# Kernel optimization log

Measured on AMD Instinct MI355X. Metric: run time of the kernel, lower is better.

The kernel has to match this reference:

```python
import jax, jax.numpy as jnp
import numpy as np

N_NODES = 100000


def gcn_conv(x, edge_index, W, b):
    """PyG GCNConv: h = x W^T; add self-loops; symmetric deg^-1/2 norm; scatter-add; + bias."""
    n = x.shape[0]
    src = jnp.concatenate([edge_index[0], jnp.arange(n)])  # self-loops appended
    dst = jnp.concatenate([edge_index[1], jnp.arange(n)])
    deg = jax.ops.segment_sum(jnp.ones_like(dst, dtype=x.dtype), dst, num_segments=n)
    dinv = jnp.where(deg > 0, jax.lax.rsqrt(deg), 0.0)
    norm = dinv[src] * dinv[dst]                             # [E+n]
    h = x @ W.T                                              # [n, out]
    msg = norm[:, None] * h[src]                             # [E+n, out] gather
    out = jax.ops.segment_sum(msg, dst, num_segments=n)      # scatter-add
    return out + b


def setup_inputs() -> dict:
    key = jax.random.key(0)
    ks = jax.random.split(key, 10)
    input_dim, gnn_hidden, tree_hidden, num_classes = 128, 64, 32, 8
    n_edges = 3200000
    x = jax.random.normal(ks[0], (N_NODES, input_dim), dtype=jnp.float32)
    edge_index = jax.random.randint(ks[1], (2, n_edges), 0, N_NODES, dtype=jnp.int64)
    # GCNConv params (PyG Linear weight is [out, in], glorot-ish scale)
    W1 = jax.random.normal(ks[2], (gnn_hidden, input_dim), dtype=jnp.float32) / np.sqrt(input_dim)
    b1 = jnp.zeros((gnn_hidden,), dtype=jnp.float32)
    W2 = jax.random.normal(ks[3], (tree_hidden, gnn_hidden), dtype=jnp.float32) / np.sqrt(gnn_hidden)
    b2 = jnp.zeros((tree_hidden,), dtype=jnp.float32)
    # SoftDecisionTree params (torch.randn init in source)
    gate_w = jax.random.normal(ks[4], (tree_hidden, tree_hidden), dtype=jnp.float32)
    gate_b = jnp.zeros((tree_hidden,), dtype=jnp.float32)
    leaf_w = jax.random.normal(ks[5], (tree_hidden, num_classes), dtype=jnp.float32)
    return {"x": x, "edge_index": edge_index, "W1": W1, "b1": b1, "W2": W2,
            "b2": b2, "gate_w": gate_w, "gate_b": gate_b, "leaf_w": leaf_w}


def reference(x, edge_index, W1, b1, W2, b2, gate_w, gate_b, leaf_w):
    h = jax.nn.relu(gcn_conv(x, edge_index, W1, b1))
    h = gcn_conv(h, edge_index, W2, b2)
    gates = jax.nn.sigmoid(h @ gate_w.T + gate_b)
    return gates @ leaf_w
```

## Files before the change

### kernel.cpp

```cpp
#include <hip/hip_runtime.h>
#include <math.h>

#define IN_DIM 128
#define H1 64
#define H2 32
#define NC 8
#define SCAN_CH 1024
#define NB_MAX 512
#define BLK 512
#define CAP 12288

typedef unsigned int u32;

__device__ __forceinline__ float bf_lo(u32 u) { return __uint_as_float(u << 16); }
__device__ __forceinline__ float bf_hi(u32 u) { return __uint_as_float(u & 0xffff0000u); }
__device__ __forceinline__ unsigned short f2b(float f) {
  u32 u = __float_as_uint(f);
  u += 0x7fffu + ((u >> 16) & 1u);
  return (unsigned short)(u >> 16);
}


__global__ __launch_bounds__(256) void k_hist(const int* __restrict__ dst,
                                              int* __restrict__ bh,
                                              int E, int EPB, int NBk) {
  __shared__ int h[NB_MAX];
  int k = blockIdx.x, tid = threadIdx.x;
  for (int i = tid; i < NBk; i += 256) h[i] = 0;
  __syncthreads();
  int st = k * EPB, en = min(E, st + EPB);
  for (int i = st + tid; i < en; i += 256)
    atomicAdd(&h[((u32)dst[i]) >> 8], 1);
  __syncthreads();
  for (int b = tid; b < NBk; b += 256) bh[b * BLK + k] = h[b];
}


__global__ __launch_bounds__(256) void k_gsc1(const int* __restrict__ A,
                                              int* __restrict__ bsum, int L) {
  int b = blockIdx.x, tid = threadIdx.x;
  int i0 = b * SCAN_CH + tid * 4;
  int s = 0;
  if (i0 + 3 < L) {
    int4 v = *(const int4*)(A + i0);
    s = v.x + v.y + v.z + v.w;
  } else {
    for (int i = i0; i < L; ++i) s += A[i];
  }
  __shared__ int red[256];
  red[tid] = s;
  __syncthreads();
  for (int d = 128; d > 0; d >>= 1) {
    if (tid < d) red[tid] += red[tid + d];
    __syncthreads();
  }
  if (tid == 0) bsum[b] = red[0];
}

__global__ __launch_bounds__(256) void k_gsc2(const int* __restrict__ bsum,
                                              int* __restrict__ bbase,
                                              int* __restrict__ S, int nbk, int L) {
  __shared__ int part[256];
  int tid = threadIdx.x;
  int chunk = (nbk + 255) / 256;
  int st = tid * chunk, en = min(st + chunk, nbk);
  int s = 0;
  for (int i = st; i < en; ++i) s += bsum[i];
  part[tid] = s;
  __syncthreads();
  for (int d = 1; d < 256; d <<= 1) {
    int t = (tid >= d) ? part[tid - d] : 0;
    __syncthreads();
    part[tid] += t;
    __syncthreads();
  }
  int base = (tid == 0) ? 0 : part[tid - 1];
  for (int i = st; i < en; ++i) { bbase[i] = base; base += bsum[i]; }
  if (tid == 255) S[L] = part[255];
}

__global__ __launch_bounds__(256) void k_gsc3(const int* __restrict__ A,
                                              const int* __restrict__ bbase,
                                              int* __restrict__ S, int L) {
  int b = blockIdx.x, tid = threadIdx.x;
  int i0 = b * SCAN_CH + tid * 4;
  int e0 = 0, e1 = 0, e2 = 0, e3 = 0;
  if (i0 + 3 < L) {
    int4 v = *(const int4*)(A + i0);
    e0 = v.x; e1 = v.y; e2 = v.z; e3 = v.w;
  } else {
    if (i0 + 0 < L) e0 = A[i0 + 0];
    if (i0 + 1 < L) e1 = A[i0 + 1];
    if (i0 + 2 < L) e2 = A[i0 + 2];
    if (i0 + 3 < L) e3 = A[i0 + 3];
  }
  __shared__ int part[256];
  part[tid] = e0 + e1 + e2 + e3;
  __syncthreads();
  for (int d = 1; d < 256; d <<= 1) {
    int t = (tid >= d) ? part[tid - d] : 0;
    __syncthreads();
    part[tid] += t;
    __syncthreads();
  }
  int base = bbase[b] + ((tid == 0) ? 0 : part[tid - 1]);
  int o0 = base, o1 = o0 + e0, o2 = o1 + e1, o3 = o2 + e2;
  if (i0 + 3 < L) {
    int4 o; o.x = o0; o.y = o1; o.z = o2; o.w = o3;
    *(int4*)(S + i0) = o;
  } else {
    if (i0 + 0 < L) S[i0 + 0] = o0;
    if (i0 + 1 < L) S[i0 + 1] = o1;
    if (i0 + 2 < L) S[i0 + 2] = o2;
    if (i0 + 3 < L) S[i0 + 3] = o3;
  }
}


__global__ __launch_bounds__(256) void k_scatter(const int* __restrict__ src,
                                                 const int* __restrict__ dst,
                                                 const int* __restrict__ S,
                                                 u32* __restrict__ packed,
                                                 int E, int EPB, int NBk) {
  __shared__ int cur[NB_MAX];
  int k = blockIdx.x, tid = threadIdx.x;
  for (int b = tid; b < NBk; b += 256) cur[b] = S[b * BLK + k];
  __syncthreads();
  int st = k * EPB, en = min(E, st + EPB);
  for (int i = st + tid; i < en; i += 256) {
    int d = dst[i];
    int b = ((u32)d) >> 8;
    int pos = atomicAdd(&cur[b], 1);
    packed[pos] = (((u32)d & 255u) << 17) | (u32)src[i];
  }
}


__global__ __launch_bounds__(256) void k_build(const u32* __restrict__ packed,
                                               const int* __restrict__ S,
                                               int* __restrict__ csr,
                                               int* __restrict__ off,
                                               float* __restrict__ dinv,
                                               int n, int NBk) {
  __shared__ int cnt[256];
  __shared__ int tmp[256];
  __shared__ int cur[256];
  __shared__ int sbuf[CAP];
  int b = blockIdx.x, tid = threadIdx.x;
  int r0 = S[b * BLK];
  int r1 = S[(b + 1) * BLK];
  int m = r1 - r0;
  cnt[tid] = 0;
  __syncthreads();
  for (int i = r0 + tid; i < r1; i += 256)
    atomicAdd(&cnt[packed[i] >> 17], 1);
  __syncthreads();
  int v = cnt[tid];
  tmp[tid] = v;
  __syncthreads();
  for (int d = 1; d < 256; d <<= 1) {
    int t = (tid >= d) ? tmp[tid - d] : 0;
    __syncthreads();
    tmp[tid] += t;
    __syncthreads();
  }
  int rel = tmp[tid] - v;
  int node = b * 256 + tid;
  if (node < n) {
    off[node] = r0 + rel;
    dinv[node] = rsqrtf((float)(v + 1));
  }
  if (b == NBk - 1 && tid == 0) off[n] = r1;
  cur[tid] = rel;
  __syncthreads();
  if (m <= CAP) {
    for (int i = r0 + tid; i < r1; i += 256) {
      u32 u = packed[i];
      int pos = atomicAdd(&cur[u >> 17], 1);
      sbuf[pos] = (int)(u & 0x1FFFFu);
    }
    __syncthreads();
    for (int j = tid; j < m; j += 256)
      csr[r0 + j] = sbuf[j];
  } else {
    for (int i = r0 + tid; i < r1; i += 256) {
      u32 u = packed[i];
      int pos = atomicAdd(&cur[u >> 17], 1);
      csr[r0 + pos] = (int)(u & 0x1FFFFu);
    }
  }
}


__global__ void k_proj1(const float4* __restrict__ x4, const float* __restrict__ W1,
                        const float* __restrict__ dinv,
                        unsigned short* __restrict__ h1p, int n) {
  __shared__ float xs[16][IN_DIM];
  __shared__ float wt[IN_DIM][H1 + 1];
  int tid = threadIdx.x;
  int row0 = blockIdx.x * 16;

  for (int i = tid; i < (H1 * IN_DIM / 4); i += 256) {
    float4 w = ((const float4*)W1)[i];
    int o = (i * 4) / IN_DIM;
    int k = (i * 4) % IN_DIM;
    wt[k + 0][o] = w.x; wt[k + 1][o] = w.y; wt[k + 2][o] = w.z; wt[k + 3][o] = w.w;
  }
  for (int i = tid; i < 16 * IN_DIM / 4; i += 256) {
    int r = (i * 4) / IN_DIM, k = (i * 4) % IN_DIM;
    int row = row0 + r;
    if (row < n)
      *((float4*)&xs[r][k]) = x4[(size_t)row * (IN_DIM / 4) + k / 4];
  }
  __syncthreads();

  int o = tid & 63, rq = tid >> 6;
  float a0 = 0.f, a1 = 0.f, a2 = 0.f, a3 = 0.f;
  for (int k = 0; k < IN_DIM; ++k) {
    float w = wt[k][o];
    a0 += xs[rq * 4 + 0][k] * w;
    a1 += xs[rq * 4 + 1][k] * w;
    a2 += xs[rq * 4 + 2][k] * w;
    a3 += xs[rq * 4 + 3][k] * w;
  }
  int r = row0 + rq * 4;
  if (r + 0 < n) h1p[(size_t)(r + 0) * H1 + o] = f2b(a0 * dinv[r + 0]);
  if (r + 1 < n) h1p[(size_t)(r + 1) * H1 + o] = f2b(a1 * dinv[r + 1]);
  if (r + 2 < n) h1p[(size_t)(r + 2) * H1 + o] = f2b(a2 * dinv[r + 2]);
  if (r + 3 < n) h1p[(size_t)(r + 3) * H1 + o] = f2b(a3 * dinv[r + 3]);
}


__global__ __launch_bounds__(256) void k_agg64_proj2(
    const u32* __restrict__ hp,
    const float* __restrict__ dinv,
    const int* __restrict__ off, const int* __restrict__ csr,
    const float* __restrict__ b1, const float* __restrict__ W2,
    unsigned short* __restrict__ h2p, int n) {
  __shared__ float wt[H1][H2 + 1];
  __shared__ float rows[4][H1];
  int tid = threadIdx.x;

  for (int i = tid; i < H2 * H1 / 4; i += 256) {
    float4 w = ((const float4*)W2)[i];
    int o = (i * 4) / H1, k = (i * 4) % H1;
    wt[k + 0][o] = w.x; wt[k + 1][o] = w.y; wt[k + 2][o] = w.z; wt[k + 3][o] = w.w;
  }

  int lane = tid & 63;
  int wv = __builtin_amdgcn_readfirstlane(tid >> 6);
  int wid0 = blockIdx.x * 4 + wv;
  int wid = wid0 < n ? wid0 : n - 1;
  int half = lane >> 5, f2 = lane & 31;

  float ax = 0.f, ay = 0.f;
  if (half == 0) {
    u32 u = hp[(size_t)wid * (H1 / 2) + f2];
    ax = bf_lo(u); ay = bf_hi(u);
  }
  int r0 = off[wid], r1 = off[wid + 1];
  int i = r0 + half;
  for (; i + 6 < r1; i += 8) {
    int s0 = csr[i + 0], s1 = csr[i + 2], s2 = csr[i + 4], s3 = csr[i + 6];
    u32 u0 = hp[(size_t)s0 * (H1 / 2) + f2];
    u32 u1 = hp[(size_t)s1 * (H1 / 2) + f2];
    u32 u2 = hp[(size_t)s2 * (H1 / 2) + f2];
    u32 u3 = hp[(size_t)s3 * (H1 / 2) + f2];
    ax += bf_lo(u0); ay += bf_hi(u0);
    ax += bf_lo(u1); ay += bf_hi(u1);
    ax += bf_lo(u2); ay += bf_hi(u2);
    ax += bf_lo(u3); ay += bf_hi(u3);
  }
  for (; i < r1; i += 2) {
    u32 u = hp[(size_t)csr[i] * (H1 / 2) + f2];
    ax += bf_lo(u);
    ay += bf_hi(u);
  }
  ax += __shfl_down(ax, 32, 64);
  ay += __shfl_down(ay, 32, 64);
  float d = dinv[wid];
  if (half == 0) {
    float2 rv;
    rv.x = fmaxf(ax * d + b1[2 * f2 + 0], 0.f);
    rv.y = fmaxf(ay * d + b1[2 * f2 + 1], 0.f);
    *(float2*)&rows[wv][2 * f2] = rv;
  }
  __syncthreads();

  int o = lane & 31;
  float a = 0.f;
#pragma unroll
  for (int k = 0; k < 32; ++k) {
    int kk = half * 32 + k;
    a += rows[wv][kk] * wt[kk][o];
  }
  a += __shfl_down(a, 32, 64);
  if (half == 0 && wid0 < n) h2p[(size_t)wid0 * H2 + o] = f2b(a * d);
}


__global__ __launch_bounds__(256) void k_agg32_tree(
    const u32* __restrict__ hp,
    const float* __restrict__ dinv,
    const int* __restrict__ off, const int* __restrict__ csr,
    const float* __restrict__ b2, const float* __restrict__ gate_w,
    const float* __restrict__ gate_b, const float* __restrict__ leaf_w,
    float* __restrict__ out, int n) {
  __shared__ float gwt[H2][H2 + 1];
  __shared__ float lws[H2][NC + 1];
  __shared__ float rowh[4][H2];
  __shared__ float rowg[4][H2];
  int tid = threadIdx.x;

  {
    float4 w = ((const float4*)gate_w)[tid];
    int j = (tid * 4) / H2, k = (tid * 4) % H2;
    gwt[k + 0][j] = w.x; gwt[k + 1][j] = w.y; gwt[k + 2][j] = w.z; gwt[k + 3][j] = w.w;
  }
  lws[tid >> 3][tid & 7] = leaf_w[tid];

  int lane = tid & 63;
  int wv = __builtin_amdgcn_readfirstlane(tid >> 6);
  int wid0 = blockIdx.x * 4 + wv;
  int wid = wid0 < n ? wid0 : n - 1;
  int q = lane >> 4, f2 = lane & 15;

  float ax = 0.f, ay = 0.f;
  if (q == 0) {
    u32 u = hp[(size_t)wid * (H2 / 2) + f2];
    ax = bf_lo(u); ay = bf_hi(u);
  }
  int r0 = off[wid], r1 = off[wid + 1];
  int i = r0 + q;
  for (; i + 12 < r1; i += 16) {
    int s0 = csr[i + 0], s1 = csr[i + 4], s2 = csr[i + 8], s3 = csr[i + 12];
    u32 u0 = hp[(size_t)s0 * (H2 / 2) + f2];
    u32 u1 = hp[(size_t)s1 * (H2 / 2) + f2];
    u32 u2 = hp[(size_t)s2 * (H2 / 2) + f2];
    u32 u3 = hp[(size_t)s3 * (H2 / 2) + f2];
    ax += bf_lo(u0); ay += bf_hi(u0);
    ax += bf_lo(u1); ay += bf_hi(u1);
    ax += bf_lo(u2); ay += bf_hi(u2);
    ax += bf_lo(u3); ay += bf_hi(u3);
  }
  for (; i < r1; i += 4) {
    u32 u = hp[(size_t)csr[i] * (H2 / 2) + f2];
    ax += bf_lo(u);
    ay += bf_hi(u);
  }
  ax += __shfl_down(ax, 32, 64); ay += __shfl_down(ay, 32, 64);
  ax += __shfl_down(ax, 16, 64); ay += __shfl_down(ay, 16, 64);
  float d = dinv[wid];
  if (lane < 16) {
    float2 rv;
    rv.x = ax * d + b2[2 * f2 + 0];
    rv.y = ay * d + b2[2 * f2 + 1];
    *(float2*)&rowh[wv][2 * f2] = rv;
  }
  __syncthreads();

  int half = lane >> 5, f = lane & 31;
  float g = 0.f;
#pragma unroll
  for (int k = 0; k < 16; ++k) {
    int kk = half * 16 + k;
    g += rowh[wv][kk] * gwt[kk][f];
  }
  g += __shfl_down(g, 32, 64);
  if (half == 0) rowg[wv][f] = 1.0f / (1.0f + __expf(-(g + gate_b[f])));
  __syncthreads();

  int c = lane & 7, gi = lane >> 3;
  float a = 0.f;
#pragma unroll
  for (int j4 = 0; j4 < 4; ++j4) {
    int jj = gi * 4 + j4;
    a += rowg[wv][jj] * lws[jj][c];
  }
  a += __shfl_down(a, 32, 64);
  a += __shfl_down(a, 16, 64);
  a += __shfl_down(a, 8, 64);
  if (lane < 8 && wid0 < n) out[(size_t)wid0 * NC + lane] = a;
}


extern "C" void kernel_launch(void* const* d_in, const int* in_sizes, int n_in,
                              void* d_out, int out_size, void* d_ws, size_t ws_size,
                              hipStream_t stream) {
  const float* x  = (const float*)d_in[0];
  const int*   ei = (const int*)d_in[1];
  const float* W1 = (const float*)d_in[2];
  const float* b1 = (const float*)d_in[3];
  const float* W2 = (const float*)d_in[4];
  const float* b2 = (const float*)d_in[5];
  const float* gw = (const float*)d_in[6];
  const float* gb = (const float*)d_in[7];
  const float* lw = (const float*)d_in[8];
  float* out = (float*)d_out;

  int n = in_sizes[0] / IN_DIM;
  int E = in_sizes[1] / 2;
  const int* src  = ei;
  const int* dstp = ei + E;

  int NBk = (n + 255) >> 8;
  int EPB = (E + BLK - 1) / BLK;
  int L   = NBk * BLK;
  int nbs = (L + SCAN_CH - 1) / SCAN_CH;

  size_t n4  = ((size_t)n + 3) & ~(size_t)3;
  size_t np4 = ((size_t)n + 1 + 3) & ~(size_t)3;
  size_t E4  = ((size_t)E + 3) & ~(size_t)3;
  size_t L4  = ((size_t)L + 1 + 3) & ~(size_t)3;
  size_t nbs4 = ((size_t)nbs + 3) & ~(size_t)3;
  char* w = (char*)d_ws;
  int* csr    = (int*)w;   w += E4 * 4;
  u32* packed = (u32*)w;   w += E4 * 4;
  int* bh     = (int*)w;   w += L4 * 4;
  int* S      = (int*)w;   w += L4 * 4;
  int* bsum   = (int*)w;   w += nbs4 * 4;
  int* bbase  = (int*)w;   w += nbs4 * 4;
  float* dinv = (float*)w; w += n4 * 4;
  int* off    = (int*)w;   w += np4 * 4;
  unsigned short* h1p = (unsigned short*)w;  w += n4 * (size_t)H1 * 2;
  unsigned short* h2p = (unsigned short*)w;

  int gw4 = (n + 3) / 4;

  k_hist<<<BLK, 256, 0, stream>>>(dstp, bh, E, EPB, NBk);
  k_gsc1<<<nbs, 256, 0, stream>>>(bh, bsum, L);
  k_gsc2<<<1, 256, 0, stream>>>(bsum, bbase, S, nbs, L);
  k_gsc3<<<nbs, 256, 0, stream>>>(bh, bbase, S, L);
  k_scatter<<<BLK, 256, 0, stream>>>(src, dstp, S, packed, E, EPB, NBk);
  k_build<<<NBk, 256, 0, stream>>>(packed, S, csr, off, dinv, n, NBk);

  k_proj1<<<(n + 15) / 16, 256, 0, stream>>>((const float4*)x, W1, dinv, h1p, n);
  k_agg64_proj2<<<gw4, 256, 0, stream>>>((const u32*)h1p, dinv, off, csr, b1, W2, h2p, n);
  k_agg32_tree<<<gw4, 256, 0, stream>>>((const u32*)h2p, dinv, off, csr, b2, gw, gb, lw, out, n);
}
```

Before: 415.7 us.

## Use 16-byte gathers and wave-cooperative CSR index loads in aggregation kernels

```diff
diff --git a/kernel.cpp b/kernel.cpp
--- a/kernel.cpp
+++ b/kernel.cpp
@@ -231,6 +231,18 @@
 }
 
 
+#define ACC8(v) do { \
+    a0 += bf_lo((v).x); a1 += bf_hi((v).x); \
+    a2 += bf_lo((v).y); a3 += bf_hi((v).y); \
+    a4 += bf_lo((v).z); a5 += bf_hi((v).z); \
+    a6 += bf_lo((v).w); a7 += bf_hi((v).w); } while (0)
+
+#define RED8(m) do { \
+    a0 += __shfl_xor(a0, m, 64); a1 += __shfl_xor(a1, m, 64); \
+    a2 += __shfl_xor(a2, m, 64); a3 += __shfl_xor(a3, m, 64); \
+    a4 += __shfl_xor(a4, m, 64); a5 += __shfl_xor(a5, m, 64); \
+    a6 += __shfl_xor(a6, m, 64); a7 += __shfl_xor(a7, m, 64); } while (0)
+
 __global__ __launch_bounds__(256) void k_agg64_proj2(
     const u32* __restrict__ hp,
     const float* __restrict__ dinv,
@@ -239,6 +251,7 @@
     unsigned short* __restrict__ h2p, int n) {
   __shared__ float wt[H1][H2 + 1];
   __shared__ float rows[4][H1];
+  __shared__ float b1s[H1];
   int tid = threadIdx.x;
 
   for (int i = tid; i < H2 * H1 / 4; i += 256) {
@@ -246,48 +259,55 @@
     int o = (i * 4) / H1, k = (i * 4) % H1;
     wt[k + 0][o] = w.x; wt[k + 1][o] = w.y; wt[k + 2][o] = w.z; wt[k + 3][o] = w.w;
   }
+  if (tid < 16) ((float4*)b1s)[tid] = ((const float4*)b1)[tid];
+  __syncthreads();
 
   int lane = tid & 63;
   int wv = __builtin_amdgcn_readfirstlane(tid >> 6);
   int wid0 = blockIdx.x * 4 + wv;
   int wid = wid0 < n ? wid0 : n - 1;
-  int half = lane >> 5, f2 = lane & 31;
-
-  float ax = 0.f, ay = 0.f;
-  if (half == 0) {
-    u32 u = hp[(size_t)wid * (H1 / 2) + f2];
-    ax = bf_lo(u); ay = bf_hi(u);
+  int g = lane >> 3, j = lane & 7;
+
+  const uint4* __restrict__ hp4 = (const uint4*)hp;
+  float a0 = 0.f, a1 = 0.f, a2 = 0.f, a3 = 0.f,
+        a4 = 0.f, a5 = 0.f, a6 = 0.f, a7 = 0.f;
+
+  if (g == 0) {
+    uint4 v = hp4[(size_t)wid * (H1 / 8) + j];
+    ACC8(v);
   }
   int r0 = off[wid], r1 = off[wid + 1];
-  int i = r0 + half;
-  for (; i + 6 < r1; i += 8) {
-    int s0 = csr[i + 0], s1 = csr[i + 2], s2 = csr[i + 4], s3 = csr[i + 6];
-    u32 u0 = hp[(size_t)s0 * (H1 / 2) + f2];
-    u32 u1 = hp[(size_t)s1 * (H1 / 2) + f2];
-    u32 u2 = hp[(size_t)s2 * (H1 / 2) + f2];
-    u32 u3 = hp[(size_t)s3 * (H1 / 2) + f2];
-    ax += bf_lo(u0); ay += bf_hi(u0);
-    ax += bf_lo(u1); ay += bf_hi(u1);
-    ax += bf_lo(u2); ay += bf_hi(u2);
-    ax += bf_lo(u3); ay += bf_hi(u3);
-  }
-  for (; i < r1; i += 2) {
-    u32 u = hp[(size_t)csr[i] * (H1 / 2) + f2];
-    ax += bf_lo(u);
-    ay += bf_hi(u);
-  }
-  ax += __shfl_down(ax, 32, 64);
-  ay += __shfl_down(ay, 32, 64);
+  for (int base = r0; base < r1; base += 32) {
+    int ci = base + (lane & 31);
+    int s = csr[min(ci, r1 - 1)];
+#pragma unroll
+    for (int it = 0; it < 4; ++it) {
+      int sv = __shfl(s, it * 8 + g, 64);
+      if (base + it * 8 + g < r1) {
+        uint4 v = hp4[(size_t)sv * (H1 / 8) + j];
+        ACC8(v);
+      }
+    }
+  }
+  RED8(8); RED8(16); RED8(32);
+
   float d = dinv[wid];
-  if (half == 0) {
-    float2 rv;
-    rv.x = fmaxf(ax * d + b1[2 * f2 + 0], 0.f);
-    rv.y = fmaxf(ay * d + b1[2 * f2 + 1], 0.f);
-    *(float2*)&rows[wv][2 * f2] = rv;
-  }
-  __syncthreads();
-
-  int o = lane & 31;
+  if (lane < 8) {
+    float4 v0, v1;
+    v0.x = fmaxf(a0 * d + b1s[8 * lane + 0], 0.f);
+    v0.y = fmaxf(a1 * d + b1s[8 * lane + 1], 0.f);
+    v0.z = fmaxf(a2 * d + b1s[8 * lane + 2], 0.f);
+    v0.w = fmaxf(a3 * d + b1s[8 * lane + 3], 0.f);
+    v1.x = fmaxf(a4 * d + b1s[8 * lane + 4], 0.f);
+    v1.y = fmaxf(a5 * d + b1s[8 * lane + 5], 0.f);
+    v1.z = fmaxf(a6 * d + b1s[8 * lane + 6], 0.f);
+    v1.w = fmaxf(a7 * d + b1s[8 * lane + 7], 0.f);
+    *(float4*)&rows[wv][8 * lane + 0] = v0;
+    *(float4*)&rows[wv][8 * lane + 4] = v1;
+  }
+  __syncthreads();
+
+  int half = lane >> 5, o = lane & 31;
   float a = 0.f;
 #pragma unroll
   for (int k = 0; k < 32; ++k) {
@@ -310,64 +330,72 @@
   __shared__ float lws[H2][NC + 1];
   __shared__ float rowh[4][H2];
   __shared__ float rowg[4][H2];
+  __shared__ float b2s[H2];
   int tid = threadIdx.x;
 
   {
     float4 w = ((const float4*)gate_w)[tid];
-    int j = (tid * 4) / H2, k = (tid * 4) % H2;
-    gwt[k + 0][j] = w.x; gwt[k + 1][j] = w.y; gwt[k + 2][j] = w.z; gwt[k + 3][j] = w.w;
+    int jj = (tid * 4) / H2, k = (tid * 4) % H2;
+    gwt[k + 0][jj] = w.x; gwt[k + 1][jj] = w.y; gwt[k + 2][jj] = w.z; gwt[k + 3][jj] = w.w;
   }
   lws[tid >> 3][tid & 7] = leaf_w[tid];
+  if (tid < 8) ((float4*)b2s)[tid] = ((const float4*)b2)[tid];
+  __syncthreads();
 
   int lane = tid & 63;
   int wv = __builtin_amdgcn_readfirstlane(tid >> 6);
   int wid0 = blockIdx.x * 4 + wv;
   int wid = wid0 < n ? wid0 : n - 1;
-  int q = lane >> 4, f2 = lane & 15;
-
-  float ax = 0.f, ay = 0.f;
-  if (q == 0) {
-    u32 u = hp[(size_t)wid * (H2 / 2) + f2];
-    ax = bf_lo(u); ay = bf_hi(u);
+  int g = lane >> 2, j = lane & 3;
+
+  const uint4* __restrict__ hp4 = (const uint4*)hp;
+  float a0 = 0.f, a1 = 0.f, a2 = 0.f, a3 = 0.f,
+        a4 = 0.f, a5 = 0.f, a6 = 0.f, a7 = 0.f;
+
+  if (g == 0) {
+    uint4 v = hp4[(size_t)wid * (H2 / 8) + j];
+    ACC8(v);
   }
   int r0 = off[wid], r1 = off[wid + 1];
-  int i = r0 + q;
-  for (; i + 12 < r1; i += 16) {
-    int s0 = csr[i + 0], s1 = csr[i + 4], s2 = csr[i + 8], s3 = csr[i + 12];
-    u32 u0 = hp[(size_t)s0 * (H2 / 2) + f2];
-    u32 u1 = hp[(size_t)s1 * (H2 / 2) + f2];
-    u32 u2 = hp[(size_t)s2 * (H2 / 2) + f2];
-    u32 u3 = hp[(size_t)s3 * (H2 / 2) + f2];
-    ax += bf_lo(u0); ay += bf_hi(u0);
-    ax += bf_lo(u1); ay += bf_hi(u1);
-    ax += bf_lo(u2); ay += bf_hi(u2);
-    ax += bf_lo(u3); ay += bf_hi(u3);
-  }
-  for (; i < r1; i += 4) {
-    u32 u = hp[(size_t)csr[i] * (H2 / 2) + f2];
-    ax += bf_lo(u);
-    ay += bf_hi(u);
-  }
-  ax += __shfl_down(ax, 32, 64); ay += __shfl_down(ay, 32, 64);
-  ax += __shfl_down(ax, 16, 64); ay += __shfl_down(ay, 16, 64);
+  for (int base = r0; base < r1; base += 32) {
+    int ci = base + (lane & 31);
+    int s = csr[min(ci, r1 - 1)];
+#pragma unroll
+    for (int it = 0; it < 2; ++it) {
+      int sv = __shfl(s, it * 16 + g, 64);
+      if (base + it * 16 + g < r1) {
+        uint4 v = hp4[(size_t)sv * (H2 / 8) + j];
+        ACC8(v);
+      }
+    }
+  }
+  RED8(4); RED8(8); RED8(16); RED8(32);
+
   float d = dinv[wid];
-  if (lane < 16) {
-    float2 rv;
-    rv.x = ax * d + b2[2 * f2 + 0];
-    rv.y = ay * d + b2[2 * f2 + 1];
-    *(float2*)&rowh[wv][2 * f2] = rv;
+  if (lane < 4) {
+    float4 v0, v1;
+    v0.x = a0 * d + b2s[8 * lane + 0];
+    v0.y = a1 * d + b2s[8 * lane + 1];
+    v0.z = a2 * d + b2s[8 * lane + 2];
+    v0.w = a3 * d + b2s[8 * lane + 3];
+    v1.x = a4 * d + b2s[8 * lane + 4];
+    v1.y = a5 * d + b2s[8 * lane + 5];
+    v1.z = a6 * d + b2s[8 * lane + 6];
+    v1.w = a7 * d + b2s[8 * lane + 7];
+    *(float4*)&rowh[wv][8 * lane + 0] = v0;
+    *(float4*)&rowh[wv][8 * lane + 4] = v1;
   }
   __syncthreads();
 
   int half = lane >> 5, f = lane & 31;
-  float g = 0.f;
+  float gacc = 0.f;
 #pragma unroll
   for (int k = 0; k < 16; ++k) {
     int kk = half * 16 + k;
-    g += rowh[wv][kk] * gwt[kk][f];
-  }
-  g += __shfl_down(g, 32, 64);
-  if (half == 0) rowg[wv][f] = 1.0f / (1.0f + __expf(-(g + gate_b[f])));
+    gacc += rowh[wv][kk] * gwt[kk][f];
+  }
+  gacc += __shfl_down(gacc, 32, 64);
+  if (half == 0) rowg[wv][f] = 1.0f / (1.0f + __expf(-(gacc + gate_b[f])));
   __syncthreads();
 
   int c = lane & 7, gi = lane >> 3;
```

Result: no change. 412.2 us (-0.9%).
